# Kernel tuning notes

Hardware: AMD Instinct MI355X
Metric: run time of the kernel (lower is better)

Reference implementation:

```python
import jax, jax.numpy as jnp
import numpy as np

B, OBS, A, T, E, H = 2048, 1024, 512, 64, 16, 64


def setup_inputs() -> dict:
    key = jax.random.key(0)
    ks = jax.random.split(key, 20)
    w = lambda k, shp, s=0.05: (jax.random.normal(k, shp, dtype=jnp.float32) * s)
    x = jax.random.normal(ks[0], (B, OBS), dtype=jnp.float32)
    action_types = jax.random.randint(ks[1], (B, A), 0, T, dtype=jnp.int32)
    # valid action counts in [1, A] so no env has an empty (all -inf) logit row
    action_counts = jax.random.randint(ks[2], (B,), 1, A + 1, dtype=jnp.int32)
    # sampled action must index a valid (unmasked) logit
    action = jnp.mod(jax.random.randint(ks[3], (B,), 0, A, dtype=jnp.int32), action_counts)
    return {
        "x": x, "action_types": action_types, "action_counts": action_counts, "action": action,
        "emb": w(ks[4], (T, E)),
        # actor_base: obs->64->64, tanh
        "W1": w(ks[5], (OBS, H)), "b1": jnp.zeros((H,), jnp.float32),
        "W2": w(ks[6], (H, H)), "b2": jnp.zeros((H,), jnp.float32),
        # action_head first linear split: [feat(64) | embed(16)] -> 64
        "Wf": w(ks[7], (H, H)), "We": w(ks[8], (E, H)), "ba": jnp.zeros((H,), jnp.float32),
        "Wo": w(ks[9], (H, 1), 0.01), "bo": jnp.zeros((1,), jnp.float32),
        # critic: obs->64->64->1, tanh
        "Wc1": w(ks[10], (OBS, H)), "bc1": jnp.zeros((H,), jnp.float32),
        "Wc2": w(ks[11], (H, H)), "bc2": jnp.zeros((H,), jnp.float32),
        "Wc3": w(ks[12], (H, 1), 1.0), "bc3": jnp.zeros((1,), jnp.float32),
    }


def reference(x, action_types, action_counts, action, emb, W1, b1, W2, b2,
              Wf, We, ba, Wo, bo, Wc1, bc1, Wc2, bc2, Wc3, bc3):
    # actor_base features [B,H]
    feats = jnp.tanh(jnp.tanh(x @ W1 + b1) @ W2 + b2)
    # ragged action scoring, padded to [B,A]:
    # combined = cat(feats_broadcast, embed(action_types)); first linear split as Wf/We
    ae = emb[action_types]                                   # [B,A,E]
    h = jnp.tanh((feats @ Wf)[:, None, :] + jnp.einsum('bae,eh->bah', ae, We) + ba)  # [B,A,H]
    scores = jnp.einsum('bah,h->ba', h, Wo[:, 0]) + bo[0]    # [B,A]
    mask = jnp.arange(A, dtype=jnp.int32)[None, :] < action_counts[:, None]
    logits = jnp.where(mask, scores, -jnp.inf)
    logp = jax.nn.log_softmax(logits, axis=-1)               # [B,A]
    log_prob = jnp.take_along_axis(logp, action[:, None].astype(jnp.int32), axis=1)[:, 0]
    p = jnp.exp(logp)
    entropy = -jnp.sum(jnp.where(mask, p * logp, 0.0), axis=-1)
    # critic value [B,1]
    value = jnp.tanh(jnp.tanh(x @ Wc1 + bc1) @ Wc2 + bc2) @ Wc3 + bc3
    return jnp.stack([log_prob, entropy, value[:, 0]], axis=-1)  # [B,3]
```

## Files before the change

### kernel.cpp

```cpp
#include <hip/hip_runtime.h>
#include <hip/hip_bf16.h>

#define B_    2048
#define OBS_  1024
#define A_    512
#define NC    128
#define NSLICE 8
#define PADK  136

typedef __attribute__((ext_vector_type(8))) short bf16x8;
typedef __attribute__((ext_vector_type(4))) float f32x4;

__device__ __forceinline__ float fast_tanh(float x) {
    return 1.0f - 2.0f / (__expf(2.0f * x) + 1.0f);
}

__device__ __forceinline__ unsigned short rne_bf16(float f) {
    union { float f; unsigned u; } v; v.f = f;
    unsigned u = v.u;
    return (unsigned short)((u + 0x7FFFu + ((u >> 16) & 1u)) >> 16);
}

__device__ __forceinline__ unsigned pack_bf16(float lo, float hi) {
    return (unsigned)rne_bf16(lo) | ((unsigned)rne_bf16(hi) << 16);
}

__device__ __forceinline__ short to_bf16(float f) {
    __hip_bfloat16 h = __float2bfloat16(f);
    return *reinterpret_cast<short*>(&h);
}

#define RL(x, k) __int_as_float(__builtin_amdgcn_readlane(__float_as_int(x), (k)))

__global__ __launch_bounds__(256) void k1_mfma(
        const float* __restrict__ x, const float* __restrict__ W1,
        const float* __restrict__ Wc1, const float* __restrict__ emb,
        const float* __restrict__ We, float* __restrict__ partials,
        float* __restrict__ embWeT) {
    __shared__ unsigned short wT[128 * PADK];
    const int tid    = threadIdx.x;
    const int mb     = blockIdx.x >> 3;
    const int kslice = blockIdx.x & 7;
    const int k0     = kslice * 128;

    {
        const int n  = tid & 127;
        const int th = tid >> 7;
        const float* src = (n < 64) ? (W1 + n) : (Wc1 + (n - 64));
        #pragma unroll
        for (int gg = 0; gg < 16; ++gg) {
            int kq = gg * 2 + th;
            int k  = k0 + kq * 4;
            float w0 = src[(size_t)(k + 0) * 64];
            float w1 = src[(size_t)(k + 1) * 64];
            float w2 = src[(size_t)(k + 2) * 64];
            float w3 = src[(size_t)(k + 3) * 64];
            unsigned long long v = (unsigned long long)pack_bf16(w0, w1)
                                 | ((unsigned long long)pack_bf16(w2, w3) << 32);
            *reinterpret_cast<unsigned long long*>(&wT[n * PADK + kq * 4]) = v;
        }
    }
    __syncthreads();

    const int w = tid >> 6;
    const int l = tid & 63;
    const int c = l & 15;
    const int g = l >> 4;

    const float* xrow = x + (size_t)(mb * 16 + c) * OBS_ + k0 + g * 8;
    const int nt0 = 2 * w, nt1 = 2 * w + 1;
    const unsigned short* bp0 = &wT[(nt0 * 16 + c) * PADK + g * 8];
    const unsigned short* bp1 = &wT[(nt1 * 16 + c) * PADK + g * 8];

    f32x4 acc0 = {0.f, 0.f, 0.f, 0.f};
    f32x4 acc1 = {0.f, 0.f, 0.f, 0.f};
    #pragma unroll
    for (int ks = 0; ks < 4; ++ks) {
        const float4* xp = (const float4*)(xrow + ks * 32);
        float4 a0 = xp[0];
        float4 a1 = xp[1];
        bf16x8 av;
        av[0] = to_bf16(a0.x); av[1] = to_bf16(a0.y);
        av[2] = to_bf16(a0.z); av[3] = to_bf16(a0.w);
        av[4] = to_bf16(a1.x); av[5] = to_bf16(a1.y);
        av[6] = to_bf16(a1.z); av[7] = to_bf16(a1.w);
        bf16x8 bv0 = *(const bf16x8*)(bp0 + ks * 32);
        bf16x8 bv1 = *(const bf16x8*)(bp1 + ks * 32);
        acc0 = __builtin_amdgcn_mfma_f32_16x16x32_bf16(av, bv0, acc0, 0, 0, 0);
        acc1 = __builtin_amdgcn_mfma_f32_16x16x32_bf16(av, bv1, acc1, 0, 0, 0);
    }

    float* pbase = partials + (size_t)kslice * B_ * NC;
    const int rbase = mb * 16 + g * 4;
    {
        int col = nt0 * 16 + c;
        #pragma unroll
        for (int r = 0; r < 4; ++r)
            pbase[(size_t)(rbase + r) * NC + col] = acc0[r];
    }
    {
        int col = nt1 * 16 + c;
        #pragma unroll
        for (int r = 0; r < 4; ++r)
            pbase[(size_t)(rbase + r) * NC + col] = acc1[r];
    }

    if (blockIdx.x < 16) {
        int idx = blockIdx.x * 256 + tid;
        int h = idx >> 6, t = idx & 63;
        float s = 0.f;
        #pragma unroll
        for (int e = 0; e < 16; ++e) s += emb[t * 16 + e] * We[e * 64 + h];
        embWeT[idx] = s;
    }
}

__global__ __launch_bounds__(256) void k2_score(
        const float* __restrict__ partials, const float* __restrict__ embWeT,
        const int* __restrict__ action_types, const int* __restrict__ action_counts,
        const int* __restrict__ action,
        const float* __restrict__ b1, const float* __restrict__ bc1,
        const float* __restrict__ W2, const float* __restrict__ b2,
        const float* __restrict__ Wf,
        const float* __restrict__ ba, const float* __restrict__ Wo,
        const float* __restrict__ bo, const float* __restrict__ Wc2,
        const float* __restrict__ bc2, const float* __restrict__ Wc3,
        const float* __restrict__ bc3, float* __restrict__ out) {
    __shared__ unsigned sW2p[32][64];
    __shared__ unsigned sWfp[32][64];
    __shared__ unsigned sWc2p[32][64];
    __shared__ unsigned sVTp[32][64];
    __shared__ int scnt[4][64];

    const int tid = threadIdx.x;
    #pragma unroll
    for (int i = 0; i < 8; ++i) {
        int idx = tid + i * 256;
        int rp = idx >> 6, hh = idx & 63;
        sW2p [rp][hh] = pack_bf16(W2 [(2 * rp) * 64 + hh], W2 [(2 * rp + 1) * 64 + hh]);
        sWfp [rp][hh] = pack_bf16(Wf [(2 * rp) * 64 + hh], Wf [(2 * rp + 1) * 64 + hh]);
        sWc2p[rp][hh] = pack_bf16(Wc2[(2 * rp) * 64 + hh], Wc2[(2 * rp + 1) * 64 + hh]);
        sVTp [rp][hh] = pack_bf16(embWeT[(2 * rp) * 64 + hh], embWeT[(2 * rp + 1) * 64 + hh]);
    }
    scnt[tid >> 6][tid & 63] = 0;
    __syncthreads();

    const int lane = tid & 63;
    const int wid  = tid >> 6;
    const int b    = blockIdx.x * 4 + wid;

    const float* pa = partials + (size_t)b * NC + lane;
    float h1v = 0.f, c1v = 0.f;
    #pragma unroll
    for (int s8 = 0; s8 < NSLICE; ++s8) {
        h1v += pa[(size_t)s8 * B_ * NC];
        c1v += pa[(size_t)s8 * B_ * NC + 64];
    }
    h1v = fast_tanh(h1v + b1[lane]);
    c1v = fast_tanh(c1v + bc1[lane]);
    const int* at_row = action_types + (size_t)b * A_;
    const int count = action_counts[b];
    const int base = lane * 8;
    int4 p0 = *reinterpret_cast<const int4*>(at_row + base);
    int4 p1 = *reinterpret_cast<const int4*>(at_row + base + 4);
    const int a_star = action[b];
    const int t_star = at_row[a_star] & 63;

    float f = b2[lane];
    #pragma unroll
    for (int kp = 0; kp < 32; ++kp) {
        unsigned pw = sW2p[kp][lane];
        f += RL(h1v, 2 * kp)     * __uint_as_float(pw << 16);
        f += RL(h1v, 2 * kp + 1) * __uint_as_float(pw & 0xffff0000u);
    }
    f = fast_tanh(f);

    float u = ba[lane];
    #pragma unroll
    for (int kp = 0; kp < 32; ++kp) {
        unsigned pw = sWfp[kp][lane];
        u += RL(f, 2 * kp)     * __uint_as_float(pw << 16);
        u += RL(f, 2 * kp + 1) * __uint_as_float(pw & 0xffff0000u);
    }

    float cc = bc2[lane];
    #pragma unroll
    for (int kp = 0; kp < 32; ++kp) {
        unsigned pw = sWc2p[kp][lane];
        cc += RL(c1v, 2 * kp)     * __uint_as_float(pw << 16);
        cc += RL(c1v, 2 * kp + 1) * __uint_as_float(pw & 0xffff0000u);
    }
    cc = fast_tanh(cc);
    float pv = cc * Wc3[lane];
    #pragma unroll
    for (int off = 32; off > 0; off >>= 1) pv += __shfl_xor(pv, off);
    const float value = pv + bc3[0];

    float s = bo[0];
    #pragma unroll
    for (int hp = 0; hp < 32; ++hp) {
        unsigned pvv = sVTp[hp][lane];
        s += fast_tanh(RL(u, 2 * hp)     + __uint_as_float(pvv << 16))         * Wo[2 * hp];
        s += fast_tanh(RL(u, 2 * hp + 1) + __uint_as_float(pvv & 0xffff0000u)) * Wo[2 * hp + 1];
    }

    int* cptr = scnt[wid];
    if (base + 0 < count) atomicAdd(&cptr[p0.x & 63], 1);
    if (base + 1 < count) atomicAdd(&cptr[p0.y & 63], 1);
    if (base + 2 < count) atomicAdd(&cptr[p0.z & 63], 1);
    if (base + 3 < count) atomicAdd(&cptr[p0.w & 63], 1);
    if (base + 4 < count) atomicAdd(&cptr[p1.x & 63], 1);
    if (base + 5 < count) atomicAdd(&cptr[p1.y & 63], 1);
    if (base + 6 < count) atomicAdd(&cptr[p1.z & 63], 1);
    if (base + 7 < count) atomicAdd(&cptr[p1.w & 63], 1);

    const int cv = cptr[lane];
    float mval = (cv > 0) ? s : -3.0e38f;
    #pragma unroll
    for (int off = 32; off > 0; off >>= 1) mval = fmaxf(mval, __shfl_xor(mval, off));
    const float e  = (float)cv * __expf(s - mval);
    float se = e, sd = e * s;
    #pragma unroll
    for (int off = 32; off > 0; off >>= 1) {
        se += __shfl_xor(se, off);
        sd += __shfl_xor(sd, off);
    }
    const float logZ    = mval + __logf(se);
    const float entropy = logZ - sd / se;
    const float logp    = __shfl(s, t_star) - logZ;

    if (lane == 0) {
        out[b * 3 + 0] = logp;
        out[b * 3 + 1] = entropy;
        out[b * 3 + 2] = value;
    }
}

extern "C" void kernel_launch(void* const* d_in, const int* in_sizes, int n_in,
                              void* d_out, int out_size, void* d_ws, size_t ws_size,
                              hipStream_t stream) {
    const float* x             = (const float*)d_in[0];
    const int*   action_types  = (const int*)  d_in[1];
    const int*   action_counts = (const int*)  d_in[2];
    const int*   action        = (const int*)  d_in[3];
    const float* emb           = (const float*)d_in[4];
    const float* W1            = (const float*)d_in[5];
    const float* b1            = (const float*)d_in[6];
    const float* W2            = (const float*)d_in[7];
    const float* b2            = (const float*)d_in[8];
    const float* Wf            = (const float*)d_in[9];
    const float* We            = (const float*)d_in[10];
    const float* ba            = (const float*)d_in[11];
    const float* Wo            = (const float*)d_in[12];
    const float* bo            = (const float*)d_in[13];
    const float* Wc1           = (const float*)d_in[14];
    const float* bc1           = (const float*)d_in[15];
    const float* Wc2           = (const float*)d_in[16];
    const float* bc2           = (const float*)d_in[17];
    const float* Wc3           = (const float*)d_in[18];
    const float* bc3           = (const float*)d_in[19];
    float* out = (float*)d_out;

    unsigned char* ws = (unsigned char*)d_ws;
    float* embWeT   = (float*)ws;
    float* partials = (float*)(ws + 16384);

    k1_mfma<<<1024, 256, 0, stream>>>(x, W1, Wc1, emb, We, partials, embWeT);
    k2_score<<<512, 256, 0, stream>>>(partials, embWeT, action_types, action_counts,
                                      action, b1, bc1, W2, b2, Wf, ba, Wo, bo,
                                      Wc2, bc2, Wc3, bc3, out);
}
```

Baseline: 28.04 us.

## Double M-tile per block in k1 and pre-pack bf16 small weights once

k1 now computes 32 rows per block instead of 16, so each transposed W1/Wc1 tile staged in LDS is reused across two M tiles and the grid is halved. The bf16 packing of W2, Wf, Wc2 and the emb@We table moves into k1, spread over 32 blocks and written to the workspace. Each of the 512 k2 blocks then just copies packed words into LDS instead of repacking from fp32. The trade is fewer, heavier k1 blocks with more accumulator registers, and a larger workspace layout.

```diff
diff --git a/kernel.cpp b/kernel.cpp
--- a/kernel.cpp
+++ b/kernel.cpp
@@ -32,15 +32,23 @@
 
 #define RL(x, k) __int_as_float(__builtin_amdgcn_readlane(__float_as_int(x), (k)))
 
+#define WS_VTP   0
+#define WS_W2P   8192
+#define WS_WFP   16384
+#define WS_WC2P  24576
+#define WS_PART  32768
+
 __global__ __launch_bounds__(256) void k1_mfma(
         const float* __restrict__ x, const float* __restrict__ W1,
         const float* __restrict__ Wc1, const float* __restrict__ emb,
-        const float* __restrict__ We, float* __restrict__ partials,
-        float* __restrict__ embWeT) {
+        const float* __restrict__ We, const float* __restrict__ W2,
+        const float* __restrict__ Wf, const float* __restrict__ Wc2,
+        unsigned char* __restrict__ ws) {
     __shared__ unsigned short wT[128 * PADK];
     const int tid    = threadIdx.x;
-    const int mb     = blockIdx.x >> 3;
-    const int kslice = blockIdx.x & 7;
+    const int bid    = blockIdx.x;
+    const int mb     = bid >> 3;
+    const int kslice = bid & 7;
     const int k0     = kslice * 128;
 
     {
@@ -67,63 +75,81 @@
     const int c = l & 15;
     const int g = l >> 4;
 
-    const float* xrow = x + (size_t)(mb * 16 + c) * OBS_ + k0 + g * 8;
+    const float* xrow0 = x + (size_t)(mb * 32 + c) * OBS_ + k0 + g * 8;
+    const float* xrow1 = xrow0 + (size_t)16 * OBS_;
     const int nt0 = 2 * w, nt1 = 2 * w + 1;
     const unsigned short* bp0 = &wT[(nt0 * 16 + c) * PADK + g * 8];
     const unsigned short* bp1 = &wT[(nt1 * 16 + c) * PADK + g * 8];
 
-    f32x4 acc0 = {0.f, 0.f, 0.f, 0.f};
-    f32x4 acc1 = {0.f, 0.f, 0.f, 0.f};
+    f32x4 acc00 = {0.f, 0.f, 0.f, 0.f};
+    f32x4 acc01 = {0.f, 0.f, 0.f, 0.f};
+    f32x4 acc10 = {0.f, 0.f, 0.f, 0.f};
+    f32x4 acc11 = {0.f, 0.f, 0.f, 0.f};
     #pragma unroll
     for (int ks = 0; ks < 4; ++ks) {
-        const float4* xp = (const float4*)(xrow + ks * 32);
-        float4 a0 = xp[0];
-        float4 a1 = xp[1];
-        bf16x8 av;
-        av[0] = to_bf16(a0.x); av[1] = to_bf16(a0.y);
-        av[2] = to_bf16(a0.z); av[3] = to_bf16(a0.w);
-        av[4] = to_bf16(a1.x); av[5] = to_bf16(a1.y);
-        av[6] = to_bf16(a1.z); av[7] = to_bf16(a1.w);
+        const float4* xp0 = (const float4*)(xrow0 + ks * 32);
+        const float4* xp1 = (const float4*)(xrow1 + ks * 32);
+        float4 a0 = xp0[0], a1 = xp0[1];
+        float4 b0 = xp1[0], b1 = xp1[1];
+        bf16x8 av0, av1;
+        av0[0] = to_bf16(a0.x); av0[1] = to_bf16(a0.y);
+        av0[2] = to_bf16(a0.z); av0[3] = to_bf16(a0.w);
+        av0[4] = to_bf16(a1.x); av0[5] = to_bf16(a1.y);
+        av0[6] = to_bf16(a1.z); av0[7] = to_bf16(a1.w);
+        av1[0] = to_bf16(b0.x); av1[1] = to_bf16(b0.y);
+        av1[2] = to_bf16(b0.z); av1[3] = to_bf16(b0.w);
+        av1[4] = to_bf16(b1.x); av1[5] = to_bf16(b1.y);
+        av1[6] = to_bf16(b1.z); av1[7] = to_bf16(b1.w);
         bf16x8 bv0 = *(const bf16x8*)(bp0 + ks * 32);
         bf16x8 bv1 = *(const bf16x8*)(bp1 + ks * 32);
-        acc0 = __builtin_amdgcn_mfma_f32_16x16x32_bf16(av, bv0, acc0, 0, 0, 0);
-        acc1 = __builtin_amdgcn_mfma_f32_16x16x32_bf16(av, bv1, acc1, 0, 0, 0);
-    }
-
-    float* pbase = partials + (size_t)kslice * B_ * NC;
-    const int rbase = mb * 16 + g * 4;
-    {
-        int col = nt0 * 16 + c;
-        #pragma unroll
-        for (int r = 0; r < 4; ++r)
-            pbase[(size_t)(rbase + r) * NC + col] = acc0[r];
-    }
-    {
-        int col = nt1 * 16 + c;
-        #pragma unroll
-        for (int r = 0; r < 4; ++r)
-            pbase[(size_t)(rbase + r) * NC + col] = acc1[r];
-    }
-
-    if (blockIdx.x < 16) {
-        int idx = blockIdx.x * 256 + tid;
-        int h = idx >> 6, t = idx & 63;
-        float s = 0.f;
-        #pragma unroll
-        for (int e = 0; e < 16; ++e) s += emb[t * 16 + e] * We[e * 64 + h];
-        embWeT[idx] = s;
+        acc00 = __builtin_amdgcn_mfma_f32_16x16x32_bf16(av0, bv0, acc00, 0, 0, 0);
+        acc01 = __builtin_amdgcn_mfma_f32_16x16x32_bf16(av0, bv1, acc01, 0, 0, 0);
+        acc10 = __builtin_amdgcn_mfma_f32_16x16x32_bf16(av1, bv0, acc10, 0, 0, 0);
+        acc11 = __builtin_amdgcn_mfma_f32_16x16x32_bf16(av1, bv1, acc11, 0, 0, 0);
+    }
+
+    float* pbase = (float*)(ws + WS_PART) + (size_t)kslice * B_ * NC;
+    const int col0 = nt0 * 16 + c;
+    const int col1 = nt1 * 16 + c;
+    const int r0   = mb * 32 + g * 4;
+    const int r1   = r0 + 16;
+    #pragma unroll
+    for (int r = 0; r < 4; ++r) {
+        pbase[(size_t)(r0 + r) * NC + col0] = acc00[r];
+        pbase[(size_t)(r0 + r) * NC + col1] = acc01[r];
+        pbase[(size_t)(r1 + r) * NC + col0] = acc10[r];
+        pbase[(size_t)(r1 + r) * NC + col1] = acc11[r];
+    }
+
+    if (bid < 32) {
+        const int job = bid >> 3;
+        const int idx = (bid & 7) * 256 + tid;
+        if (job == 0) {
+            int hp = idx >> 6, t = idx & 63;
+            float s0 = 0.f, s1 = 0.f;
+            #pragma unroll
+            for (int e = 0; e < 16; ++e) {
+                float ev = emb[t * 16 + e];
+                s0 += ev * We[e * 64 + 2 * hp];
+                s1 += ev * We[e * 64 + 2 * hp + 1];
+            }
+            ((unsigned*)(ws + WS_VTP))[idx] = pack_bf16(s0, s1);
+        } else {
+            const float* src = (job == 1) ? W2 : (job == 2) ? Wf : Wc2;
+            unsigned* dst = (unsigned*)(ws + ((job == 1) ? WS_W2P : (job == 2) ? WS_WFP : WS_WC2P));
+            int rp = idx >> 6, hh = idx & 63;
+            dst[idx] = pack_bf16(src[(2 * rp) * 64 + hh], src[(2 * rp + 1) * 64 + hh]);
+        }
     }
 }
 
 __global__ __launch_bounds__(256) void k2_score(
-        const float* __restrict__ partials, const float* __restrict__ embWeT,
+        const unsigned char* __restrict__ ws,
         const int* __restrict__ action_types, const int* __restrict__ action_counts,
         const int* __restrict__ action,
         const float* __restrict__ b1, const float* __restrict__ bc1,
-        const float* __restrict__ W2, const float* __restrict__ b2,
-        const float* __restrict__ Wf,
-        const float* __restrict__ ba, const float* __restrict__ Wo,
-        const float* __restrict__ bo, const float* __restrict__ Wc2,
+        const float* __restrict__ b2, const float* __restrict__ ba,
+        const float* __restrict__ Wo, const float* __restrict__ bo,
         const float* __restrict__ bc2, const float* __restrict__ Wc3,
         const float* __restrict__ bc3, float* __restrict__ out) {
     __shared__ unsigned sW2p[32][64];
@@ -133,14 +159,19 @@
     __shared__ int scnt[4][64];
 
     const int tid = threadIdx.x;
-    #pragma unroll
-    for (int i = 0; i < 8; ++i) {
-        int idx = tid + i * 256;
-        int rp = idx >> 6, hh = idx & 63;
-        sW2p [rp][hh] = pack_bf16(W2 [(2 * rp) * 64 + hh], W2 [(2 * rp + 1) * 64 + hh]);
-        sWfp [rp][hh] = pack_bf16(Wf [(2 * rp) * 64 + hh], Wf [(2 * rp + 1) * 64 + hh]);
-        sWc2p[rp][hh] = pack_bf16(Wc2[(2 * rp) * 64 + hh], Wc2[(2 * rp + 1) * 64 + hh]);
-        sVTp [rp][hh] = pack_bf16(embWeT[(2 * rp) * 64 + hh], embWeT[(2 * rp + 1) * 64 + hh]);
+    {
+        const unsigned* gV = (const unsigned*)(ws + WS_VTP);
+        const unsigned* g2 = (const unsigned*)(ws + WS_W2P);
+        const unsigned* gF = (const unsigned*)(ws + WS_WFP);
+        const unsigned* gC = (const unsigned*)(ws + WS_WC2P);
+        #pragma unroll
+        for (int i = 0; i < 8; ++i) {
+            int idx = tid + i * 256;
+            ((unsigned*)sVTp)[idx]  = gV[idx];
+            ((unsigned*)sW2p)[idx]  = g2[idx];
+            ((unsigned*)sWfp)[idx]  = gF[idx];
+            ((unsigned*)sWc2p)[idx] = gC[idx];
+        }
     }
     scnt[tid >> 6][tid & 63] = 0;
     __syncthreads();
@@ -149,7 +180,7 @@
     const int wid  = tid >> 6;
     const int b    = blockIdx.x * 4 + wid;
 
-    const float* pa = partials + (size_t)b * NC + lane;
+    const float* pa = (const float*)(ws + WS_PART) + (size_t)b * NC + lane;
     float h1v = 0.f, c1v = 0.f;
     #pragma unroll
     for (int s8 = 0; s8 < NSLICE; ++s8) {
@@ -260,13 +291,9 @@
     const float* Wc3           = (const float*)d_in[18];
     const float* bc3           = (const float*)d_in[19];
     float* out = (float*)d_out;
-
     unsigned char* ws = (unsigned char*)d_ws;
-    float* embWeT   = (float*)ws;
-    float* partials = (float*)(ws + 16384);
-
-    k1_mfma<<<1024, 256, 0, stream>>>(x, W1, Wc1, emb, We, partials, embWeT);
-    k2_score<<<512, 256, 0, stream>>>(partials, embWeT, action_types, action_counts,
-                                      action, b1, bc1, W2, b2, Wf, ba, Wo, bo,
-                                      Wc2, bc2, Wc3, bc3, out);
-}
+
+    k1_mfma<<<512, 256, 0, stream>>>(x, W1, Wc1, emb, We, W2, Wf, Wc2, ws);
+    k2_score<<<512, 256, 0, stream>>>(ws, action_types, action_counts, action,
+                                      b1, bc1, b2, ba, Wo, bo, bc2, Wc3, bc3, out);
+}
```

Result: faster. 26.71 us (-4.7%).
